# Performance work log

Hardware: AMD Instinct MI355X
Metric: run time of the kernel (lower is better)

The kernel has to match this reference:

```python
import jax, jax.numpy as jnp
import numpy as np

N_ATOMS = 4096
N_ANGLES = 200000


def setup_inputs() -> dict:
    key = jax.random.key(0)
    k1, k2, k3, k4, k5 = jax.random.split(key, 5)
    # pairwise unit direction vectors [N, N, 3]
    vec = jax.random.normal(k1, (N_ATOMS, N_ATOMS, 3), dtype=jnp.float32)
    vec = vec / jnp.linalg.norm(vec, axis=-1, keepdims=True)
    # pairwise distances [N, N], strictly positive
    dist = jax.random.uniform(k2, (N_ATOMS, N_ATOMS), dtype=jnp.float32) * 2.0 + 0.5
    # angle triplets [A, 3]
    coord_idx = jax.random.randint(k3, (N_ANGLES, 3), 0, N_ATOMS)
    # per-angle parameters: k0 (force const) and theta0 (equilibrium angle, rad)
    k0 = jax.random.uniform(k4, (N_ANGLES,), dtype=jnp.float32) * 100.0
    theta0 = jax.random.uniform(k5, (N_ANGLES,), dtype=jnp.float32) * np.float32(np.pi)
    params = jnp.stack([k0, theta0], axis=1)
    forces_out = jnp.zeros((N_ATOMS, 3), dtype=jnp.float32)
    return {
        "dist_mat": dist,
        "vector_mat": vec,
        "forces_out": forces_out,
        "params": params,
        "coord_idx": coord_idx,
        "calc_energy": 1,
        "calc_forces": 1,
    }


def reference(dist_mat, vector_mat, forces_out, params, coord_idx, calc_energy, calc_forces):
    k0 = params[:, 0]
    theta0 = params[:, 1]
    a1 = coord_idx[:, 0]
    a2 = coord_idx[:, 1]
    a3 = coord_idx[:, 2]

    vec21 = vector_mat[a2, a1]            # [A, 3]
    vec23 = vector_mat[a2, a3]            # [A, 3]
    dist21 = dist_mat[a2, a1]             # [A]
    dist23 = dist_mat[a2, a3]             # [A]

    cos_theta = jnp.clip(jnp.sum(vec21 * vec23, axis=1), -1.0, 1.0)
    theta = jnp.arccos(cos_theta)
    delta_theta = theta - theta0

    if calc_energy:
        energy = jnp.sum(k0 * delta_theta * delta_theta)
    else:
        energy = jnp.zeros([1], dtype=forces_out.dtype)

    forces = forces_out
    if calc_forces:
        sin_theta = jnp.sqrt(1.0 - cos_theta * cos_theta)
        # matches torch nan_to_num(nan=0.0): zero out coef where sin_theta == 0
        coef = jnp.where(sin_theta > 0.0,
                         -2.0 * k0 * delta_theta / jnp.maximum(sin_theta, 1e-12),
                         0.0)
        force0 = coef[:, None] * (cos_theta[:, None] * vec21 - vec23) / dist21[:, None]
        force2 = coef[:, None] * (cos_theta[:, None] * vec23 - vec21) / dist23[:, None]
        force1 = -(force0 + force2)
        forces = forces.at[a1].add(force0).at[a2].add(force1).at[a3].add(force2)

    return energy, forces
```

## Files before the change

kernel.cpp:

```cpp
#include <hip/hip_runtime.h>


__global__ void init_out_kernel(float* __restrict__ out,
                                const float* __restrict__ forces0,
                                int nf) {
    int j = blockIdx.x * blockDim.x + threadIdx.x;
    if (j == 0) out[0] = 0.0f;
    if (j < nf) out[1 + j] = forces0[j];
}

#define NB 256
#define NT 1024

__global__ void __launch_bounds__(NT)
angle_fused_kernel(const float*  __restrict__ dist,
                   const float*  __restrict__ vec,
                   const float2* __restrict__ params,
                   const int*    __restrict__ cidx,
                   const int*    __restrict__ ce_p,
                   const int*    __restrict__ cf_p,
                   float* __restrict__ out,
                   int n_atoms, int n_angles) {
    extern __shared__ float s_f[];
    __shared__ float s_e;
    const int nf  = n_atoms * 3;
    const int tid = threadIdx.x;
    const int b   = blockIdx.x;

    for (int j = tid; j < nf; j += NT) s_f[j] = 0.0f;
    if (tid == 0) s_e = 0.0f;
    __syncthreads();

    const int ce = ce_p[0];
    const int cf = cf_p[0];

    const int i0 = (int)(((long)b * n_angles) / NB);
    const int i1 = (int)(((long)(b + 1) * n_angles) / NB);
    const int i  = i0 + tid;

    float e_acc = 0.0f;
    if (i < i1) {
        const int a1 = cidx[3 * i + 0];
        const int a2 = cidx[3 * i + 1];
        const int a3 = cidx[3 * i + 2];
        const float2 kt = params[i];

        const unsigned row = (unsigned)a2 * (unsigned)n_atoms;
        const unsigned b21 = row + (unsigned)a1;
        const unsigned b23 = row + (unsigned)a3;
        const float* __restrict__ p21 = vec + 3u * b21;
        const float* __restrict__ p23 = vec + 3u * b23;

        const float v21x = p21[0], v21y = p21[1], v21z = p21[2];
        const float v23x = p23[0], v23y = p23[1], v23z = p23[2];
        const float d21 = dist[b21];
        const float d23 = dist[b23];

        float c = v21x * v23x + v21y * v23y + v21z * v23z;
        c = fminf(1.0f, fmaxf(-1.0f, c));
        const float th  = acosf(c);
        const float dth = th - kt.y;

        if (ce) e_acc = kt.x * dth * dth;

        if (cf) {
            const float s2 = fmaxf(0.0f, 1.0f - c * c);
            const float s  = sqrtf(s2);
            const float coef = (s > 0.0f) ? (-2.0f * kt.x * dth / fmaxf(s, 1e-12f)) : 0.0f;
            const float i21 = coef / d21;
            const float i23 = coef / d23;

            const float f0x = i21 * (c * v21x - v23x);
            const float f0y = i21 * (c * v21y - v23y);
            const float f0z = i21 * (c * v21z - v23z);
            const float f2x = i23 * (c * v23x - v21x);
            const float f2y = i23 * (c * v23y - v21y);
            const float f2z = i23 * (c * v23z - v21z);

            atomicAdd(&s_f[a1 * 3 + 0], f0x);
            atomicAdd(&s_f[a1 * 3 + 1], f0y);
            atomicAdd(&s_f[a1 * 3 + 2], f0z);
            atomicAdd(&s_f[a2 * 3 + 0], -(f0x + f2x));
            atomicAdd(&s_f[a2 * 3 + 1], -(f0y + f2y));
            atomicAdd(&s_f[a2 * 3 + 2], -(f0z + f2z));
            atomicAdd(&s_f[a3 * 3 + 0], f2x);
            atomicAdd(&s_f[a3 * 3 + 1], f2y);
            atomicAdd(&s_f[a3 * 3 + 2], f2z);
        }
    }

    for (int off = 32; off > 0; off >>= 1)
        e_acc += __shfl_down(e_acc, off, 64);
    if ((tid & 63) == 0) atomicAdd(&s_e, e_acc);
    __syncthreads();

    if (ce && tid == 0) atomicAdd(&out[0], s_e);

    if (cf) {
        const int base = (b * (nf / NB)) % nf;
        for (int jj = tid; jj < nf; jj += NT) {
            int j = jj + base;
            if (j >= nf) j -= nf;
            const float v = s_f[j];
            if (v != 0.0f) atomicAdd(&out[1 + j], v);
        }
    }
}

extern "C" void kernel_launch(void* const* d_in, const int* in_sizes, int n_in,
                              void* d_out, int out_size, void* d_ws, size_t ws_size,
                              hipStream_t stream) {
    const float*  dist    = (const float*)d_in[0];
    const float*  vec     = (const float*)d_in[1];
    const float*  forces0 = (const float*)d_in[2];
    const float2* params  = (const float2*)d_in[3];
    const int*    cidx    = (const int*)d_in[4];
    const int*    ce_p    = (const int*)d_in[5];
    const int*    cf_p    = (const int*)d_in[6];
    float* out = (float*)d_out;

    const int n_atoms  = in_sizes[2] / 3;
    const int n_angles = in_sizes[4] / 3;
    const int nf = n_atoms * 3;

    init_out_kernel<<<(nf + 1 + 255) / 256, 256, 0, stream>>>(out, forces0, nf);

    const size_t lds_bytes = (size_t)nf * sizeof(float);
    angle_fused_kernel<<<NB, NT, lds_bytes, stream>>>(dist, vec, params, cidx,
                                                      ce_p, cf_p, out,
                                                      n_atoms, n_angles);
}
```

Baseline: 301.5 us.

## Replace global atomic force merge with per-block workspace and deterministic reduce kernel

```diff
diff --git a/kernel.cpp b/kernel.cpp
--- a/kernel.cpp
+++ b/kernel.cpp
@@ -1,5 +1,8 @@
 #include <hip/hip_runtime.h>
 
+
+#define NB 256
+#define NT 1024
 
 __global__ void init_out_kernel(float* __restrict__ out,
                                 const float* __restrict__ forces0,
@@ -9,9 +12,7 @@
     if (j < nf) out[1 + j] = forces0[j];
 }
 
-#define NB 256
-#define NT 1024
-
+template <bool USE_WS>
 __global__ void __launch_bounds__(NT)
 angle_fused_kernel(const float*  __restrict__ dist,
                    const float*  __restrict__ vec,
@@ -20,6 +21,8 @@
                    const int*    __restrict__ ce_p,
                    const int*    __restrict__ cf_p,
                    float* __restrict__ out,
+                   float* __restrict__ ws_f,
+                   float* __restrict__ ws_e,
                    int n_atoms, int n_angles) {
     extern __shared__ float s_f[];
     __shared__ float s_e;
@@ -94,17 +97,63 @@
     if ((tid & 63) == 0) atomicAdd(&s_e, e_acc);
     __syncthreads();
 
-    if (ce && tid == 0) atomicAdd(&out[0], s_e);
-
-    if (cf) {
-        const int base = (b * (nf / NB)) % nf;
-        for (int jj = tid; jj < nf; jj += NT) {
-            int j = jj + base;
-            if (j >= nf) j -= nf;
-            const float v = s_f[j];
-            if (v != 0.0f) atomicAdd(&out[1 + j], v);
+    if constexpr (USE_WS) {
+        float* __restrict__ wp = ws_f + (size_t)b * nf;
+        const float4* __restrict__ s4 = (const float4*)s_f;
+        float4* __restrict__ w4 = (float4*)wp;
+        const int nf4 = nf >> 2;
+        for (int q = tid; q < nf4; q += NT) w4[q] = s4[q];
+        for (int j = (nf4 << 2) + tid; j < nf; j += NT) wp[j] = s_f[j];
+        if (tid == 0) ws_e[b] = s_e;
+    } else {
+        if (ce && tid == 0) atomicAdd(&out[0], s_e);
+        if (cf) {
+            const int base = (b * (nf / NB)) % nf;
+            for (int jj = tid; jj < nf; jj += NT) {
+                int j = jj + base;
+                if (j >= nf) j -= nf;
+                const float v = s_f[j];
+                if (v != 0.0f) atomicAdd(&out[1 + j], v);
+            }
         }
     }
+}
+
+__global__ void __launch_bounds__(256)
+reduce_kernel(const float* __restrict__ ws_f,
+              const float* __restrict__ ws_e,
+              const float* __restrict__ forces0,
+              const int*   __restrict__ ce_p,
+              float* __restrict__ out,
+              int nf) {
+    const int t  = threadIdx.x;
+    const int jj = t & 63;
+    const int bg = t >> 6;
+    const int j  = blockIdx.x * 64 + jj;
+
+    __shared__ float s_p[4][64];
+    __shared__ float s_e;
+
+    float acc = 0.0f;
+    if (j < nf) {
+        const float* __restrict__ p = ws_f + (size_t)(bg * 64) * nf + j;
+        #pragma unroll 16
+        for (int b = 0; b < 64; ++b) acc += p[(size_t)b * nf];
+    }
+    s_p[bg][jj] = acc;
+
+    float e = (blockIdx.x == 0) ? ws_e[t] : 0.0f;
+    if (t == 0) s_e = 0.0f;
+    __syncthreads();
+
+    if (blockIdx.x == 0) {
+        for (int off = 32; off > 0; off >>= 1) e += __shfl_down(e, off, 64);
+        if ((t & 63) == 0) atomicAdd(&s_e, e);
+    }
+    if (bg == 0 && j < nf)
+        out[1 + j] = forces0[j] + s_p[0][jj] + s_p[1][jj] + s_p[2][jj] + s_p[3][jj];
+    __syncthreads();
+    if (blockIdx.x == 0 && t == 0) out[0] = ce_p[0] ? s_e : 0.0f;
 }
 
 extern "C" void kernel_launch(void* const* d_in, const int* in_sizes, int n_in,
@@ -123,10 +172,22 @@
     const int n_angles = in_sizes[4] / 3;
     const int nf = n_atoms * 3;
 
-    init_out_kernel<<<(nf + 1 + 255) / 256, 256, 0, stream>>>(out, forces0, nf);
+    const size_t lds_bytes = (size_t)nf * sizeof(float);
+    const size_t ws_need = ((size_t)NB * nf + NB) * sizeof(float);
 
-    const size_t lds_bytes = (size_t)nf * sizeof(float);
-    angle_fused_kernel<<<NB, NT, lds_bytes, stream>>>(dist, vec, params, cidx,
-                                                      ce_p, cf_p, out,
-                                                      n_atoms, n_angles);
+    if (d_ws != nullptr && ws_size >= ws_need) {
+        float* ws_f = (float*)d_ws;
+        float* ws_e = ws_f + (size_t)NB * nf;
+        angle_fused_kernel<true><<<NB, NT, lds_bytes, stream>>>(
+            dist, vec, params, cidx, ce_p, cf_p, out, ws_f, ws_e,
+            n_atoms, n_angles);
+        const int rblocks = (nf + 63) / 64;
+        reduce_kernel<<<rblocks, 256, 0, stream>>>(ws_f, ws_e, forces0,
+                                                   ce_p, out, nf);
+    } else {
+        init_out_kernel<<<(nf + 1 + 255) / 256, 256, 0, stream>>>(out, forces0, nf);
+        angle_fused_kernel<false><<<NB, NT, lds_bytes, stream>>>(
+            dist, vec, params, cidx, ce_p, cf_p, out, nullptr, nullptr,
+            n_atoms, n_angles);
+    }
 }
```

New measurement: 296.5 us. No clear change (-1.7%).

## Replace global force atomics with bf16 per-block partials and reduction kernel

Applied to the files above, without the earlier changes.

```diff
diff --git a/kernel.cpp b/kernel.cpp
--- a/kernel.cpp
+++ b/kernel.cpp
@@ -1,5 +1,20 @@
 #include <hip/hip_runtime.h>
 
+
+#define NB 256
+#define NT 1024
+
+__device__ __forceinline__ unsigned pack_bf16x2(float a, float b) {
+    unsigned ua = __float_as_uint(a);
+    unsigned ub = __float_as_uint(b);
+    ua = (ua + 0x7FFFu + ((ua >> 16) & 1u)) >> 16;
+    ub = (ub + 0x7FFFu + ((ub >> 16) & 1u)) >> 16;
+    return ua | (ub << 16);
+}
+__device__ __forceinline__ float2 unpack_bf16x2(unsigned p) {
+    return make_float2(__uint_as_float(p << 16),
+                       __uint_as_float(p & 0xFFFF0000u));
+}
 
 __global__ void init_out_kernel(float* __restrict__ out,
                                 const float* __restrict__ forces0,
@@ -9,9 +24,7 @@
     if (j < nf) out[1 + j] = forces0[j];
 }
 
-#define NB 256
-#define NT 1024
-
+template <bool USE_WS>
 __global__ void __launch_bounds__(NT)
 angle_fused_kernel(const float*  __restrict__ dist,
                    const float*  __restrict__ vec,
@@ -19,7 +32,9 @@
                    const int*    __restrict__ cidx,
                    const int*    __restrict__ ce_p,
                    const int*    __restrict__ cf_p,
-                   float* __restrict__ out,
+                   float*    __restrict__ out,
+                   unsigned* __restrict__ ws16,
+                   float*    __restrict__ ws_e,
                    int n_atoms, int n_angles) {
     extern __shared__ float s_f[];
     __shared__ float s_e;
@@ -27,35 +42,49 @@
     const int tid = threadIdx.x;
     const int b   = blockIdx.x;
 
-    for (int j = tid; j < nf; j += NT) s_f[j] = 0.0f;
-    if (tid == 0) s_e = 0.0f;
-    __syncthreads();
-
-    const int ce = ce_p[0];
-    const int cf = cf_p[0];
-
     const int i0 = (int)(((long)b * n_angles) / NB);
     const int i1 = (int)(((long)(b + 1) * n_angles) / NB);
     const int i  = i0 + tid;
-
-    float e_acc = 0.0f;
-    if (i < i1) {
-        const int a1 = cidx[3 * i + 0];
-        const int a2 = cidx[3 * i + 1];
-        const int a3 = cidx[3 * i + 2];
-        const float2 kt = params[i];
-
+    const bool active = (i < i1);
+
+    int a1 = 0, a2 = 0, a3 = 0;
+    float2 kt = make_float2(0.0f, 0.0f);
+    if (active) {
+        a1 = cidx[3 * i + 0];
+        a2 = cidx[3 * i + 1];
+        a3 = cidx[3 * i + 2];
+        kt = params[i];
+    }
+
+    {
+        float4* __restrict__ s4 = (float4*)s_f;
+        const int nf4 = nf >> 2;
+        for (int q = tid; q < nf4; q += NT) s4[q] = make_float4(0.f, 0.f, 0.f, 0.f);
+        for (int j = (nf4 << 2) + tid; j < nf; j += NT) s_f[j] = 0.0f;
+        if (tid == 0) s_e = 0.0f;
+    }
+
+    const int ce = ce_p[0];
+    const int cf = cf_p[0];
+
+    float v21x = 0.f, v21y = 0.f, v21z = 0.f, d21 = 1.f;
+    float v23x = 0.f, v23y = 0.f, v23z = 0.f, d23 = 1.f;
+    if (active) {
         const unsigned row = (unsigned)a2 * (unsigned)n_atoms;
         const unsigned b21 = row + (unsigned)a1;
         const unsigned b23 = row + (unsigned)a3;
         const float* __restrict__ p21 = vec + 3u * b21;
         const float* __restrict__ p23 = vec + 3u * b23;
-
-        const float v21x = p21[0], v21y = p21[1], v21z = p21[2];
-        const float v23x = p23[0], v23y = p23[1], v23z = p23[2];
-        const float d21 = dist[b21];
-        const float d23 = dist[b23];
-
+        v21x = p21[0]; v21y = p21[1]; v21z = p21[2];
+        v23x = p23[0]; v23y = p23[1]; v23z = p23[2];
+        d21 = dist[b21];
+        d23 = dist[b23];
+    }
+
+    __syncthreads();
+
+    float e_acc = 0.0f;
+    if (active) {
         float c = v21x * v23x + v21y * v23y + v21z * v23z;
         c = fminf(1.0f, fmaxf(-1.0f, c));
         const float th  = acosf(c);
@@ -94,17 +123,70 @@
     if ((tid & 63) == 0) atomicAdd(&s_e, e_acc);
     __syncthreads();
 
-    if (ce && tid == 0) atomicAdd(&out[0], s_e);
-
-    if (cf) {
-        const int base = (b * (nf / NB)) % nf;
-        for (int jj = tid; jj < nf; jj += NT) {
-            int j = jj + base;
-            if (j >= nf) j -= nf;
-            const float v = s_f[j];
-            if (v != 0.0f) atomicAdd(&out[1 + j], v);
+    if constexpr (USE_WS) {
+        const int nf2 = nf >> 1;
+        unsigned* __restrict__ wp = ws16 + (size_t)b * nf2;
+        for (int q = tid; q < nf2; q += NT)
+            wp[q] = pack_bf16x2(s_f[2 * q], s_f[2 * q + 1]);
+        if (tid == 0) ws_e[b] = s_e;
+    } else {
+        if (ce && tid == 0) atomicAdd(&out[0], s_e);
+        if (cf) {
+            const int base = (b * (nf / NB)) % nf;
+            for (int jj = tid; jj < nf; jj += NT) {
+                int j = jj + base;
+                if (j >= nf) j -= nf;
+                const float v = s_f[j];
+                if (v != 0.0f) atomicAdd(&out[1 + j], v);
+            }
         }
     }
+}
+
+__global__ void __launch_bounds__(256)
+reduce_bf16_kernel(const unsigned* __restrict__ ws16,
+                   const float*    __restrict__ ws_e,
+                   const float*    __restrict__ forces0,
+                   const int*      __restrict__ ce_p,
+                   float* __restrict__ out,
+                   int nf2) {
+    const int t  = threadIdx.x;
+    const int jj = t & 63;
+    const int bg = t >> 6;
+    const int j2 = blockIdx.x * 64 + jj;
+
+    __shared__ float2 s_p[4][64];
+    __shared__ float  s_e;
+
+    float ax = 0.0f, ay = 0.0f;
+    if (j2 < nf2) {
+        const unsigned* __restrict__ p = ws16 + (size_t)(bg * 64) * nf2 + j2;
+        #pragma unroll 16
+        for (int b = 0; b < 64; ++b) {
+            const float2 v = unpack_bf16x2(p[(size_t)b * nf2]);
+            ax += v.x; ay += v.y;
+        }
+    }
+    s_p[bg][jj] = make_float2(ax, ay);
+
+    float e = (blockIdx.x == 0) ? ws_e[t] : 0.0f;
+    if (t == 0) s_e = 0.0f;
+    __syncthreads();
+
+    if (blockIdx.x == 0) {
+        for (int off = 32; off > 0; off >>= 1) e += __shfl_down(e, off, 64);
+        if ((t & 63) == 0) atomicAdd(&s_e, e);
+    }
+    if (bg == 0 && j2 < nf2) {
+        const float2 f0 = ((const float2*)forces0)[j2];
+        float sx = 0.0f, sy = 0.0f;
+        #pragma unroll
+        for (int g = 0; g < 4; ++g) { sx += s_p[g][jj].x; sy += s_p[g][jj].y; }
+        out[1 + 2 * j2]     = f0.x + sx;
+        out[1 + 2 * j2 + 1] = f0.y + sy;
+    }
+    __syncthreads();
+    if (blockIdx.x == 0 && t == 0) out[0] = ce_p[0] ? s_e : 0.0f;
 }
 
 extern "C" void kernel_launch(void* const* d_in, const int* in_sizes, int n_in,
@@ -121,12 +203,29 @@
 
     const int n_atoms  = in_sizes[2] / 3;
     const int n_angles = in_sizes[4] / 3;
-    const int nf = n_atoms * 3;
-
-    init_out_kernel<<<(nf + 1 + 255) / 256, 256, 0, stream>>>(out, forces0, nf);
+    const int nf  = n_atoms * 3;
+    const int nf2 = nf >> 1;
 
     const size_t lds_bytes = (size_t)nf * sizeof(float);
-    angle_fused_kernel<<<NB, NT, lds_bytes, stream>>>(dist, vec, params, cidx,
-                                                      ce_p, cf_p, out,
-                                                      n_atoms, n_angles);
-}
+    const size_t ws_need   = ((size_t)NB * nf2 + NB) * sizeof(unsigned);
+
+    const bool main_ok = (d_ws != nullptr) && (ws_size >= ws_need) &&
+                         ((nf & 1) == 0) && (n_angles <= NB * NT) &&
+                         (lds_bytes <= 160 * 1024 - 1024);
+
+    if (main_ok) {
+        unsigned* ws16 = (unsigned*)d_ws;
+        float*    ws_e = (float*)(ws16 + (size_t)NB * nf2);
+        angle_fused_kernel<true><<<NB, NT, lds_bytes, stream>>>(
+            dist, vec, params, cidx, ce_p, cf_p, out, ws16, ws_e,
+            n_atoms, n_angles);
+        const int rblocks = (nf2 + 63) / 64;
+        reduce_bf16_kernel<<<rblocks, 256, 0, stream>>>(ws16, ws_e, forces0,
+                                                        ce_p, out, nf2);
+    } else {
+        init_out_kernel<<<(nf + 1 + 255) / 256, 256, 0, stream>>>(out, forces0, nf);
+        angle_fused_kernel<false><<<NB, NT, lds_bytes, stream>>>(
+            dist, vec, params, cidx, ce_p, cf_p, out, nullptr, nullptr,
+            n_atoms, n_angles);
+    }
+}
```

New measurement: 299.8 us. Within noise of the previous version (-0.6%).
